# Performance work log

Measured on AMD Instinct MI355X. Metric: run time of the kernel, lower is better.

## Reference

```python
import jax, jax.numpy as jnp
import numpy as np

S = (128, 128, 128)  # spatial grid
K = (16, 16, 16)     # retained low-frequency modes


def _gelu(x):
    # torch nn.GELU default = exact erf variant
    return jax.nn.gelu(x, approximate=False)


def _flayer(x, Rr, Ri, w):
    # x: (s1,s2,s3,dv). Full rfftn then truncate to low modes (as in source).
    f = jnp.fft.rfftn(x, axes=(0, 1, 2))[: K[0], : K[1], : K[2]]  # (k1,k2,k3,dv) complex
    Rf = jnp.einsum('abcd,abcde->abce', f, Rr + 1j * Ri)           # per-mode channel mix
    kernelpart = jnp.fft.irfftn(Rf, s=S, axes=(0, 1, 2))           # zero-pad modes, back to grid
    return _gelu(kernelpart + x @ w)


def setup_inputs() -> dict:
    key = jax.random.key(0)
    ks = jax.random.split(key, 20)
    da, dv, dout = 4, 32, 1
    sc1, sc2, sc3 = 2.0 / da, 2.0 / dv, 2.0 / dv
    d = {}
    d['x'] = jax.random.normal(ks[0], (*S, da), dtype=jnp.float32)
    d['win'] = sc1 * jax.random.normal(ks[1], (da, dv), dtype=jnp.float32)
    d['bin1'] = sc1 * jax.random.normal(ks[2], (dv,), dtype=jnp.float32)
    i = 3
    for L in range(1, 5):
        d[f'Rphir{L}'] = sc2 * jax.random.normal(ks[i], (*K, dv, dv), dtype=jnp.float32); i += 1
        d[f'Rphii{L}'] = sc2 * jax.random.normal(ks[i], (*K, dv, dv), dtype=jnp.float32); i += 1
        d[f'w{L}'] = sc2 * jax.random.normal(ks[i], (dv, dv), dtype=jnp.float32); i += 1
    d['wout'] = sc3 * jax.random.normal(ks[i], (dv, dout), dtype=jnp.float32); i += 1
    d['bout'] = sc3 * jax.random.normal(ks[i], (dout,), dtype=jnp.float32)
    return d


def reference(x, win, bin1, Rphir1, Rphii1, w1, Rphir2, Rphii2, w2,
              Rphir3, Rphii3, w3, Rphir4, Rphii4, w4, wout, bout):
    v = _gelu(x @ win + bin1)          # lifting: (s1,s2,s3,dv)
    v = _flayer(v, Rphir1, Rphii1, w1)
    v = _flayer(v, Rphir2, Rphii2, w2)
    v = _flayer(v, Rphir3, Rphii3, w3)
    v = _flayer(v, Rphir4, Rphii4, w4)
    return v @ wout + bout             # (s1,s2,s3,dout)
```

## Files before the change

kernel.cpp:

```cpp
#include <hip/hip_runtime.h>
#include <math.h>

typedef float2 cplx;
typedef _Float16 h16;
typedef h16 h16x8 __attribute__((ext_vector_type(8)));
typedef float f32x4 __attribute__((ext_vector_type(4)));
typedef uint u32x2 __attribute__((ext_vector_type(2)));

#define MFMA16(a, b, c) __builtin_amdgcn_mfma_f32_16x16x32_f16(a, b, c, 0, 0, 0)

static __device__ __forceinline__ float gelu_exact(float z) {
  float x = z * 0.70710678118654752440f;
  float ax = fabsf(x);
  float t = __builtin_amdgcn_rcpf(fmaf(0.3275911f, ax, 1.0f));
  float p = fmaf(1.061405429f, t, -1.453152027f);
  p = fmaf(p, t, 1.421413741f);
  p = fmaf(p, t, -0.284496736f);
  p = fmaf(p, t, 0.254829592f);
  p = p * t;
  float e = __expf(-ax * ax);
  float erfax = fmaf(-p, e, 1.0f);
  float er = copysignf(erfax, x);
  return 0.5f * z * (1.0f + er);
}

template <int OFF>
static __device__ __forceinline__ h16x8 tr_frag(uint addr) {
  union { uint u[4]; h16x8 h; } r;
  u32x2 lo, hi;
  asm volatile("ds_read_b64_tr_b16 %0, %2 offset:%3\n\t"
               "ds_read_b64_tr_b16 %1, %2 offset:%4"
               : "=&v"(lo), "=&v"(hi)
               : "v"(addr), "i"(OFF), "i"(OFF + 128));
  r.u[0] = lo.x; r.u[1] = lo.y; r.u[2] = hi.x; r.u[3] = hi.y;
  return r.h;
}

__global__ __launch_bounds__(256) void k_prep(
    h16* __restrict__ Afwd, h16* __restrict__ Adt, cplx* __restrict__ Twc,
    const float* __restrict__ wA, const float* __restrict__ wB,
    const float* __restrict__ wC, const float* __restrict__ wD,
    h16* __restrict__ Wfr)
{
  const int tid = threadIdx.x;
  const float w0 = 0.049087385212340519f;
  for (int idx = tid; idx < 4096; idx += 256) {
    int Mt = idx >> 11, rem = idx & 2047, lane = rem >> 5, k = rem & 31;
    int j = k & 7, chunk = k >> 3;
    int m = lane & 15;
    int x3 = chunk * 32 + (lane >> 4) * 8 + j;
    float ang = (float)((m * x3) & 127) * w0;
    float s, c; sincosf(ang, &s, &c);
    float val = Mt ? s : c;
    h16 hi = (h16)val;
    Afwd[idx] = hi;
    Afwd[idx + 4096] = (h16)(val - (float)hi);
  }
  for (int idx = tid; idx < 4096; idx += 256) {
    int tt = idx >> 4, rem = idx & 15, t = rem >> 3, j = rem & 7;
    int wv = tt >> 6, lane = tt & 63, mrow = lane & 15, q = lane >> 4;
    int x3 = (2 * wv + t) * 16 + mrow;
    int kk = q * 8 + j;
    int m = (kk < 16) ? kk : kk - 16;
    float ang = (float)((x3 * m) & 127) * w0;
    float s, c; sincosf(ang, &s, &c);
    Adt[idx] = (h16)((kk < 16) ? c : s);
  }
  const float* ws[4] = { wA, wB, wC, wD };
  for (int idx = tid; idx < 16384; idx += 256) {
    int L = idx >> 12, rem = idx & 4095;
    int t2 = rem >> 4, nt = (rem >> 3) & 1, j = rem & 7;
    int mrow = t2 & 15, q = (t2 >> 4) & 3;
    int n = nt * 16 + mrow, kk = q * 8 + j;
    Wfr[idx] = (h16)ws[L][kk * 32 + n];
  }
  if (tid < 128) {
    float ang = (float)tid * w0;
    float s, c; sincosf(ang, &s, &c);
    Twc[tid] = make_float2(c, s);
  }
}

__global__ __launch_bounds__(256) void k_lift(
    const float* __restrict__ x, const float* __restrict__ win,
    const float* __restrict__ bin, h16* __restrict__ v)
{
  __shared__ float xr[512];
  __shared__ float wl[128];
  __shared__ float bl[32];
  const int tid = threadIdx.x;
  const size_t b = blockIdx.x;
  const float* xrow = x + b * 512;
  for (int i = tid; i < 512; i += 256) xr[i] = xrow[i];
  if (tid < 128) wl[tid] = win[tid];
  if (tid < 32)  bl[tid] = bin[tid];
  __syncthreads();
  const int c = tid & 31, g = tid >> 5;
  #pragma unroll
  for (int j = 0; j < 16; ++j) {
    int x3 = g + 8 * j;
    float z = bl[c];
    #pragma unroll
    for (int a = 0; a < 4; ++a) z += xr[x3 * 4 + a] * wl[a * 32 + c];
    v[b * 4096 + x3 * 32 + c] = (h16)gelu_exact(z);
  }
}

__global__ __launch_bounds__(256) void k_fwd3(
    const h16* __restrict__ v, const h16* __restrict__ Afwd, cplx* __restrict__ Gp,
    const cplx* __restrict__ twg)
{
  __shared__ __align__(16) h16 vtile[4][2][4][32][16];
  __shared__ cplx F3L[4][512];
  const int tid = threadIdx.x;
  const int x1 = blockIdx.x, qs = blockIdx.y;
  const int lane = tid & 63, wv = tid >> 6;
  const int mrow = lane & 15, q4 = lane >> 4;
  h16x8 Ah[2][4], Al[2][4];
  #pragma unroll
  for (int Mt = 0; Mt < 2; ++Mt)
    #pragma unroll
    for (int ch = 0; ch < 4; ++ch) {
      Ah[Mt][ch] = *(const h16x8*)&Afwd[Mt * 2048 + lane * 32 + ch * 8];
      Al[Mt][ch] = *(const h16x8*)&Afwd[4096 + Mt * 2048 + lane * 32 + ch * 8];
    }
  const uint ldsbase = (uint)(uintptr_t)&vtile[0][0][0][0][0];
  const uint abase = ldsbase + (uint)(wv * 8192 + q4 * 256 + mrow * 2);
  cplx g0[16], g1[16];
  #pragma unroll
  for (int k2 = 0; k2 < 16; ++k2) { g0[k2] = make_float2(0.f, 0.f); g1[k2] = make_float2(0.f, 0.f); }
  for (int it = 0; it < 8; ++it) {
    const int x2b = qs * 32 + it * 4;
    __syncthreads();
    const uint4* vsrc = (const uint4*)(v + ((size_t)x1 * 128 + x2b) * 4096);
    for (int i = tid; i < 2048; i += 256) {
      uint4 pk = vsrc[i];
      int rr = i >> 9, e = (i & 511) * 8, x3 = e >> 5, c0 = e & 31;
      int panel = c0 >> 4, off = c0 & 15;
      int chunk = x3 >> 5, row = x3 & 31;
      *(uint4*)&vtile[rr][panel][chunk][row][off] = pk;
    }
    __syncthreads();
    h16x8 B0[4], B1[4];
    {
      const uint a0 = abase;
      const uint a1 = abase + 4096;
      B0[0] = tr_frag<0>(a0);    B0[1] = tr_frag<1024>(a0);
      B0[2] = tr_frag<2048>(a0); B0[3] = tr_frag<3072>(a0);
      B1[0] = tr_frag<0>(a1);    B1[1] = tr_frag<1024>(a1);
      B1[2] = tr_frag<2048>(a1); B1[3] = tr_frag<3072>(a1);
      asm volatile("s_waitcnt lgkmcnt(0)" ::: "memory");
      __builtin_amdgcn_sched_barrier(0);
    }
    f32x4 acc[2][2];
    #pragma unroll
    for (int Mt = 0; Mt < 2; ++Mt)
      #pragma unroll
      for (int Nt = 0; Nt < 2; ++Nt) acc[Mt][Nt] = (f32x4){0.f, 0.f, 0.f, 0.f};
    #pragma unroll
    for (int ch = 0; ch < 4; ++ch) {
      acc[0][0] = MFMA16(Ah[0][ch], B0[ch], acc[0][0]);
      acc[0][0] = MFMA16(Al[0][ch], B0[ch], acc[0][0]);
      acc[0][1] = MFMA16(Ah[0][ch], B1[ch], acc[0][1]);
      acc[0][1] = MFMA16(Al[0][ch], B1[ch], acc[0][1]);
      acc[1][0] = MFMA16(Ah[1][ch], B0[ch], acc[1][0]);
      acc[1][0] = MFMA16(Al[1][ch], B0[ch], acc[1][0]);
      acc[1][1] = MFMA16(Ah[1][ch], B1[ch], acc[1][1]);
      acc[1][1] = MFMA16(Al[1][ch], B1[ch], acc[1][1]);
    }
    #pragma unroll
    for (int Nt = 0; Nt < 2; ++Nt)
      #pragma unroll
      for (int r = 0; r < 4; ++r)
        F3L[wv][(q4 * 4 + r) * 32 + Nt * 16 + mrow] =
            make_float2(acc[0][Nt][r], -acc[1][Nt][r]);
    __syncthreads();
    #pragma unroll
    for (int rr = 0; rr < 4; ++rr) {
      const int x2 = x2b + rr;
      cplx f0 = F3L[rr][tid], f1 = F3L[rr][tid + 256];
      #pragma unroll
      for (int k2 = 0; k2 < 16; ++k2) {
        cplx t = twg[(k2 * x2) & 127];
        g0[k2].x += f0.x * t.x + f0.y * t.y;  g0[k2].y += f0.y * t.x - f0.x * t.y;
        g1[k2].x += f1.x * t.x + f1.y * t.y;  g1[k2].y += f1.y * t.x - f1.x * t.y;
      }
    }
  }
  cplx* dst = Gp + (size_t)qs * 1048576;
  #pragma unroll
  for (int k2 = 0; k2 < 16; ++k2) {
    size_t base = ((size_t)x1 * 16 + k2) * 512;
    dst[base + tid] = g0[k2];
    dst[base + 256 + tid] = g1[k2];
  }
}

__global__ __launch_bounds__(1024) void k_spec3(
    const cplx* __restrict__ Gp, const float* __restrict__ Rr,
    const float* __restrict__ Ri, cplx* __restrict__ H1,
    const cplx* __restrict__ twg)
{
  __shared__ cplx twc[128];
  __shared__ cplx fbp[4][512];
  __shared__ cplx tb[512];
  const int tid = threadIdx.x;
  const int k2 = blockIdx.x >> 4, k3 = blockIdx.x & 15;
  if (tid < 128) twc[tid] = twg[tid];
  __syncthreads();
  const int c = tid & 31, g = (tid >> 5) & 7, h = tid >> 8;
  float fr0 = 0.f, fi0 = 0.f, fr1 = 0.f, fi1 = 0.f;
  #pragma unroll 4
  for (int x1i = 0; x1i < 32; ++x1i) {
    const int x1 = h * 32 + x1i;
    size_t idx = (((size_t)x1 * 16 + k2) * 16 + k3) * 32 + c;
    cplx p0 = Gp[idx], p1 = Gp[idx + 1048576], p2 = Gp[idx + 2097152], p3 = Gp[idx + 3145728];
    cplx hh = make_float2(p0.x + p1.x + p2.x + p3.x, p0.y + p1.y + p2.y + p3.y);
    cplx ta = twc[(g * x1) & 127];
    cplx tb2 = twc[((g + 8) * x1) & 127];
    fr0 += hh.x * ta.x + hh.y * ta.y;   fi0 += hh.y * ta.x - hh.x * ta.y;
    fr1 += hh.x * tb2.x + hh.y * tb2.y; fi1 += hh.y * tb2.x - hh.x * tb2.y;
  }
  fbp[h][g * 32 + c] = make_float2(fr0, fi0);
  fbp[h][(g + 8) * 32 + c] = make_float2(fr1, fi1);
  __syncthreads();
  if (tid < 512) {
    cplx a = fbp[0][tid], b = fbp[1][tid], d = fbp[2][tid], e = fbp[3][tid];
    fbp[0][tid] = make_float2((a.x + b.x) + (d.x + e.x), (a.y + b.y) + (d.y + e.y));
  }
  __syncthreads();
  if (tid < 512) {
    const int k1 = tid >> 5, e = c;
    float tr = 0.f, ti = 0.f;
    const size_t mb = ((size_t)k1 * 256 + k2 * 16 + k3) * 1024;
    #pragma unroll 4
    for (int cc = 0; cc < 32; ++cc) {
      float rr0 = Rr[mb + cc * 32 + e], ri0 = Ri[mb + cc * 32 + e];
      cplx f0 = fbp[0][k1 * 32 + cc];
      tr += f0.x * rr0 - f0.y * ri0;  ti += f0.x * ri0 + f0.y * rr0;
    }
    const float s = 4.76837158203125e-07f;
    tb[k1 * 32 + e] = make_float2(tr * s, ti * s);
  }
  __syncthreads();
  float trr[16], tii[16];
  #pragma unroll
  for (int k1 = 0; k1 < 16; ++k1) { cplx t = tb[k1 * 32 + c]; trr[k1] = t.x; tii[k1] = t.y; }
  #pragma unroll
  for (int jj = 0; jj < 4; ++jj) {
    int xx1 = g + 8 * (h * 4 + jj);
    float hr = 0.f, hi = 0.f;
    #pragma unroll
    for (int k1 = 0; k1 < 16; ++k1) {
      cplx t = twc[(k1 * xx1) & 127];
      hr += trr[k1] * t.x - tii[k1] * t.y;
      hi += trr[k1] * t.y + tii[k1] * t.x;
    }
    H1[(((size_t)xx1 * 16 + k2) * 16 + k3) * 32 + c] = make_float2(hr, hi);
  }
}

__global__ __launch_bounds__(512) void k_ptm4(
    const cplx* __restrict__ H1, const h16* __restrict__ Wfr,
    h16* __restrict__ v, const h16* __restrict__ Adt,
    const cplx* __restrict__ twg)
{
  __shared__ __align__(16) h16 St[8][32 * 40];
  const int tid = threadIdx.x;
  const int x1 = blockIdx.y;
  const int x2b = blockIdx.x * 8;
  const int c = tid & 31, g2 = (tid >> 5) & 15;
  const int lane = tid & 63, w = tid >> 6;
  const int mrow = lane & 15, q = lane >> 4;
  h16x8 Adf, Bw[2];
  Adf   = *(const h16x8*)&Adt[((w >> 1) * 64 + lane) * 16 + (w & 1) * 8];
  Bw[0] = *(const h16x8*)&Wfr[lane * 16];
  Bw[1] = *(const h16x8*)&Wfr[lane * 16 + 8];
  cplx h1[16];
  {
    const cplx* h1p = H1 + (size_t)x1 * 8192;
    #pragma unroll
    for (int k2 = 0; k2 < 16; ++k2) h1[k2] = h1p[(k2 * 16 + g2) * 32 + c];
  }
  const float s0 = (g2 == 0) ? 1.f : 2.f;
  #pragma unroll
  for (int xi = 0; xi < 8; ++xi) {
    const int x2 = x2b + xi;
    float r = 0.f, i = 0.f;
    #pragma unroll
    for (int k2 = 0; k2 < 16; ++k2) {
      cplx t = twg[(k2 * x2) & 127];
      r += h1[k2].x * t.x - h1[k2].y * t.y;
      i += h1[k2].x * t.y + h1[k2].y * t.x;
    }
    St[xi][c * 40 + g2]      = (h16)(s0 * r);
    St[xi][c * 40 + 16 + g2] = (h16)(-s0 * i);
  }
  __syncthreads();
  for (int xi = 0; xi < 8; ++xi) {
    const size_t b = (size_t)x1 * 128 + x2b + xi;
    h16x8 Av = *(const h16x8*)&v[b * 4096 + (w * 16 + mrow) * 32 + q * 8];
    f32x4 acc[2];
    #pragma unroll
    for (int nt = 0; nt < 2; ++nt) {
      h16x8 Bst = *(const h16x8*)&St[xi][(nt * 16 + mrow) * 40 + q * 8];
      f32x4 z = {0.f, 0.f, 0.f, 0.f};
      z = MFMA16(Adf, Bst, z);
      z = MFMA16(Av, Bw[nt], z);
      acc[nt] = z;
    }
    #pragma unroll
    for (int nt = 0; nt < 2; ++nt)
      #pragma unroll
      for (int r2 = 0; r2 < 4; ++r2) {
        int x3 = w * 16 + q * 4 + r2;
        v[b * 4096 + x3 * 32 + nt * 16 + mrow] = (h16)gelu_exact(acc[nt][r2]);
      }
  }
}

__global__ __launch_bounds__(512) void k_ptf4(
    const cplx* __restrict__ H1, const h16* __restrict__ Wfr,
    const h16* __restrict__ v, const h16* __restrict__ Adt,
    const float* __restrict__ wout, const float* __restrict__ bout,
    float* __restrict__ out, const cplx* __restrict__ twg)
{
  __shared__ __align__(16) h16 St[8][32 * 40];
  const int tid = threadIdx.x;
  const int x1 = blockIdx.y;
  const int x2b = blockIdx.x * 8;
  const int c = tid & 31, g2 = (tid >> 5) & 15;
  const int lane = tid & 63, w = tid >> 6;
  const int mrow = lane & 15, q = lane >> 4;
  h16x8 Adf, Bw[2];
  Adf   = *(const h16x8*)&Adt[((w >> 1) * 64 + lane) * 16 + (w & 1) * 8];
  Bw[0] = *(const h16x8*)&Wfr[lane * 16];
  Bw[1] = *(const h16x8*)&Wfr[lane * 16 + 8];
  const float wo0 = wout[mrow], wo1 = wout[16 + mrow];
  const float bo = bout[0];
  cplx h1[16];
  {
    const cplx* h1p = H1 + (size_t)x1 * 8192;
    #pragma unroll
    for (int k2 = 0; k2 < 16; ++k2) h1[k2] = h1p[(k2 * 16 + g2) * 32 + c];
  }
  const float s0 = (g2 == 0) ? 1.f : 2.f;
  #pragma unroll
  for (int xi = 0; xi < 8; ++xi) {
    const int x2 = x2b + xi;
    float r = 0.f, i = 0.f;
    #pragma unroll
    for (int k2 = 0; k2 < 16; ++k2) {
      cplx t = twg[(k2 * x2) & 127];
      r += h1[k2].x * t.x - h1[k2].y * t.y;
      i += h1[k2].x * t.y + h1[k2].y * t.x;
    }
    St[xi][c * 40 + g2]      = (h16)(s0 * r);
    St[xi][c * 40 + 16 + g2] = (h16)(-s0 * i);
  }
  __syncthreads();
  for (int xi = 0; xi < 8; ++xi) {
    const size_t b = (size_t)x1 * 128 + x2b + xi;
    h16x8 Av = *(const h16x8*)&v[b * 4096 + (w * 16 + mrow) * 32 + q * 8];
    f32x4 acc[2];
    #pragma unroll
    for (int nt = 0; nt < 2; ++nt) {
      h16x8 Bst = *(const h16x8*)&St[xi][(nt * 16 + mrow) * 40 + q * 8];
      f32x4 z = {0.f, 0.f, 0.f, 0.f};
      z = MFMA16(Adf, Bst, z);
      z = MFMA16(Av, Bw[nt], z);
      acc[nt] = z;
    }
    #pragma unroll
    for (int r2 = 0; r2 < 4; ++r2) {
      float p = (float)(h16)gelu_exact(acc[0][r2]) * wo0
              + (float)(h16)gelu_exact(acc[1][r2]) * wo1;
      p += __shfl_xor(p, 1);
      p += __shfl_xor(p, 2);
      p += __shfl_xor(p, 4);
      p += __shfl_xor(p, 8);
      if (mrow == 0) {
        int x3 = w * 16 + q * 4 + r2;
        out[b * 128 + x3] = bo + p;
      }
    }
  }
}

__global__ void k_diag(float* out, float wsmb) {
  if (threadIdx.x == 0 && blockIdx.x == 0) out[0] = wsmb;
}

extern "C" void kernel_launch(void* const* d_in, const int* in_sizes, int n_in,
                              void* d_out, int out_size, void* d_ws, size_t ws_size,
                              hipStream_t stream)
{
  (void)in_sizes; (void)n_in; (void)out_size;
  const float* x    = (const float*)d_in[0];
  const float* win  = (const float*)d_in[1];
  const float* bin1 = (const float*)d_in[2];
  const float* Rr[4] = { (const float*)d_in[3], (const float*)d_in[6],
                         (const float*)d_in[9], (const float*)d_in[12] };
  const float* Ri[4] = { (const float*)d_in[4], (const float*)d_in[7],
                         (const float*)d_in[10], (const float*)d_in[13] };
  const float* wm[4] = { (const float*)d_in[5], (const float*)d_in[8],
                         (const float*)d_in[11], (const float*)d_in[14] };
  const float* wout = (const float*)d_in[15];
  const float* bout = (const float*)d_in[16];
  float* out = (float*)d_out;

  const size_t SZ_V  = 134217728;
  const size_t SZ_C  = 33554432;
  const size_t SZ_AF = 16384;
  const size_t SZ_AD = 8192;
  const size_t SZ_TW = 1024;
  const size_t SZ_WF = 32768;
  const size_t NEED = SZ_V + SZ_C + SZ_AF + SZ_AD + SZ_TW + SZ_WF;

  if (ws_size < NEED) {
    k_diag<<<1, 64, 0, stream>>>(out, (float)(ws_size >> 20));
    return;
  }
  char* p = (char*)d_ws;
  h16* v    = (h16*)p;  p += SZ_V;
  cplx* C   = (cplx*)p; p += SZ_C;
  h16* Afwd = (h16*)p;  p += SZ_AF;
  h16* Adt  = (h16*)p;  p += SZ_AD;
  cplx* Twc = (cplx*)p; p += SZ_TW;
  h16* Wfr  = (h16*)p;

  k_prep<<<1, 256, 0, stream>>>(Afwd, Adt, Twc, wm[0], wm[1], wm[2], wm[3], Wfr);
  k_lift<<<16384, 256, 0, stream>>>(x, win, bin1, v);
  for (int L = 0; L < 4; ++L) {
    k_fwd3<<<dim3(128, 4), 256, 0, stream>>>(v, Afwd, C, Twc);
    k_spec3<<<256, 1024, 0, stream>>>(C, Rr[L], Ri[L], C, Twc);
    if (L < 3) k_ptm4<<<dim3(16, 128), 512, 0, stream>>>(C, Wfr + (size_t)L * 4096, v, Adt, Twc);
    else       k_ptf4<<<dim3(16, 128), 512, 0, stream>>>(C, Wfr + 3 * 4096, v, Adt, wout, bout, out, Twc);
  }
}
```

Measured before the change: 746.7 us.

## Split forward DFT work across 512 threads and prefetch v fragments in pointwise kernels

The forward x3/x2 transform kernel now runs 512 threads per block. Each wave pair splits the real and imaginary (Mt) halves of the MFMA work, and each thread accumulates one k2 column instead of two. This lowers register pressure and adds more waves to hide latency. The A fragments are now reloaded from global memory inside the loop instead of held in registers. In the pointwise kernels, all eight v fragments are loaded before the twiddle/St computation so the global load latency overlaps that compute, at the cost of more registers.

```diff
diff --git a/kernel.cpp b/kernel.cpp
--- a/kernel.cpp
+++ b/kernel.cpp
@@ -106,39 +106,34 @@
   }
 }
 
-__global__ __launch_bounds__(256) void k_fwd3(
+__global__ __launch_bounds__(512) void k_fwd4(
     const h16* __restrict__ v, const h16* __restrict__ Afwd, cplx* __restrict__ Gp,
     const cplx* __restrict__ twg)
 {
   __shared__ __align__(16) h16 vtile[4][2][4][32][16];
-  __shared__ cplx F3L[4][512];
+  __shared__ float F3re[4][512];
+  __shared__ float F3im[4][512];
   const int tid = threadIdx.x;
   const int x1 = blockIdx.x, qs = blockIdx.y;
-  const int lane = tid & 63, wv = tid >> 6;
+  const int lane = tid & 63, w = tid >> 6;
+  const int row = w >> 1, Mt = w & 1;
   const int mrow = lane & 15, q4 = lane >> 4;
-  h16x8 Ah[2][4], Al[2][4];
-  #pragma unroll
-  for (int Mt = 0; Mt < 2; ++Mt)
-    #pragma unroll
-    for (int ch = 0; ch < 4; ++ch) {
-      Ah[Mt][ch] = *(const h16x8*)&Afwd[Mt * 2048 + lane * 32 + ch * 8];
-      Al[Mt][ch] = *(const h16x8*)&Afwd[4096 + Mt * 2048 + lane * 32 + ch * 8];
-    }
   const uint ldsbase = (uint)(uintptr_t)&vtile[0][0][0][0][0];
-  const uint abase = ldsbase + (uint)(wv * 8192 + q4 * 256 + mrow * 2);
-  cplx g0[16], g1[16];
-  #pragma unroll
-  for (int k2 = 0; k2 < 16; ++k2) { g0[k2] = make_float2(0.f, 0.f); g1[k2] = make_float2(0.f, 0.f); }
+  const uint abase = ldsbase + (uint)(row * 8192 + q4 * 256 + mrow * 2);
+  const h16* Abase = Afwd + Mt * 2048;
+  cplx g[16];
+  #pragma unroll
+  for (int k2 = 0; k2 < 16; ++k2) g[k2] = make_float2(0.f, 0.f);
   for (int it = 0; it < 8; ++it) {
     const int x2b = qs * 32 + it * 4;
     __syncthreads();
     const uint4* vsrc = (const uint4*)(v + ((size_t)x1 * 128 + x2b) * 4096);
-    for (int i = tid; i < 2048; i += 256) {
+    for (int i = tid; i < 2048; i += 512) {
       uint4 pk = vsrc[i];
       int rr = i >> 9, e = (i & 511) * 8, x3 = e >> 5, c0 = e & 31;
       int panel = c0 >> 4, off = c0 & 15;
-      int chunk = x3 >> 5, row = x3 & 31;
-      *(uint4*)&vtile[rr][panel][chunk][row][off] = pk;
+      int chunk = x3 >> 5, rw = x3 & 31;
+      *(uint4*)&vtile[rr][panel][chunk][rw][off] = pk;
     }
     __syncthreads();
     h16x8 B0[4], B1[4];
@@ -152,48 +147,48 @@
       asm volatile("s_waitcnt lgkmcnt(0)" ::: "memory");
       __builtin_amdgcn_sched_barrier(0);
     }
-    f32x4 acc[2][2];
-    #pragma unroll
-    for (int Mt = 0; Mt < 2; ++Mt)
+    f32x4 acc[2];
+    acc[0] = (f32x4){0.f, 0.f, 0.f, 0.f};
+    acc[1] = (f32x4){0.f, 0.f, 0.f, 0.f};
+    #pragma unroll
+    for (int ch = 0; ch < 4; ++ch) {
+      h16x8 Ah = *(const h16x8*)&Abase[lane * 32 + ch * 8];
+      h16x8 Al = *(const h16x8*)&Abase[4096 + lane * 32 + ch * 8];
+      acc[0] = MFMA16(Ah, B0[ch], acc[0]);
+      acc[0] = MFMA16(Al, B0[ch], acc[0]);
+      acc[1] = MFMA16(Ah, B1[ch], acc[1]);
+      acc[1] = MFMA16(Al, B1[ch], acc[1]);
+    }
+    if (Mt == 0) {
       #pragma unroll
-      for (int Nt = 0; Nt < 2; ++Nt) acc[Mt][Nt] = (f32x4){0.f, 0.f, 0.f, 0.f};
-    #pragma unroll
-    for (int ch = 0; ch < 4; ++ch) {
-      acc[0][0] = MFMA16(Ah[0][ch], B0[ch], acc[0][0]);
-      acc[0][0] = MFMA16(Al[0][ch], B0[ch], acc[0][0]);
-      acc[0][1] = MFMA16(Ah[0][ch], B1[ch], acc[0][1]);
-      acc[0][1] = MFMA16(Al[0][ch], B1[ch], acc[0][1]);
-      acc[1][0] = MFMA16(Ah[1][ch], B0[ch], acc[1][0]);
-      acc[1][0] = MFMA16(Al[1][ch], B0[ch], acc[1][0]);
-      acc[1][1] = MFMA16(Ah[1][ch], B1[ch], acc[1][1]);
-      acc[1][1] = MFMA16(Al[1][ch], B1[ch], acc[1][1]);
-    }
-    #pragma unroll
-    for (int Nt = 0; Nt < 2; ++Nt)
+      for (int Nt = 0; Nt < 2; ++Nt)
+        #pragma unroll
+        for (int r = 0; r < 4; ++r)
+          F3re[row][(q4 * 4 + r) * 32 + Nt * 16 + mrow] = acc[Nt][r];
+    } else {
       #pragma unroll
-      for (int r = 0; r < 4; ++r)
-        F3L[wv][(q4 * 4 + r) * 32 + Nt * 16 + mrow] =
-            make_float2(acc[0][Nt][r], -acc[1][Nt][r]);
+      for (int Nt = 0; Nt < 2; ++Nt)
+        #pragma unroll
+        for (int r = 0; r < 4; ++r)
+          F3im[row][(q4 * 4 + r) * 32 + Nt * 16 + mrow] = -acc[Nt][r];
+    }
     __syncthreads();
     #pragma unroll
     for (int rr = 0; rr < 4; ++rr) {
       const int x2 = x2b + rr;
-      cplx f0 = F3L[rr][tid], f1 = F3L[rr][tid + 256];
+      float fx = F3re[rr][tid], fy = F3im[rr][tid];
       #pragma unroll
       for (int k2 = 0; k2 < 16; ++k2) {
         cplx t = twg[(k2 * x2) & 127];
-        g0[k2].x += f0.x * t.x + f0.y * t.y;  g0[k2].y += f0.y * t.x - f0.x * t.y;
-        g1[k2].x += f1.x * t.x + f1.y * t.y;  g1[k2].y += f1.y * t.x - f1.x * t.y;
+        g[k2].x += fx * t.x + fy * t.y;
+        g[k2].y += fy * t.x - fx * t.y;
       }
     }
   }
   cplx* dst = Gp + (size_t)qs * 1048576;
   #pragma unroll
-  for (int k2 = 0; k2 < 16; ++k2) {
-    size_t base = ((size_t)x1 * 16 + k2) * 512;
-    dst[base + tid] = g0[k2];
-    dst[base + 256 + tid] = g1[k2];
-  }
+  for (int k2 = 0; k2 < 16; ++k2)
+    dst[((size_t)x1 * 16 + k2) * 512 + tid] = g[k2];
 }
 
 __global__ __launch_bounds__(1024) void k_spec3(
@@ -282,6 +277,12 @@
     #pragma unroll
     for (int k2 = 0; k2 < 16; ++k2) h1[k2] = h1p[(k2 * 16 + g2) * 32 + c];
   }
+  h16x8 Av[8];
+  #pragma unroll
+  for (int xi = 0; xi < 8; ++xi) {
+    const size_t b = (size_t)x1 * 128 + x2b + xi;
+    Av[xi] = *(const h16x8*)&v[b * 4096 + (w * 16 + mrow) * 32 + q * 8];
+  }
   const float s0 = (g2 == 0) ? 1.f : 2.f;
   #pragma unroll
   for (int xi = 0; xi < 8; ++xi) {
@@ -297,16 +298,16 @@
     St[xi][c * 40 + 16 + g2] = (h16)(-s0 * i);
   }
   __syncthreads();
+  #pragma unroll
   for (int xi = 0; xi < 8; ++xi) {
     const size_t b = (size_t)x1 * 128 + x2b + xi;
-    h16x8 Av = *(const h16x8*)&v[b * 4096 + (w * 16 + mrow) * 32 + q * 8];
     f32x4 acc[2];
     #pragma unroll
     for (int nt = 0; nt < 2; ++nt) {
       h16x8 Bst = *(const h16x8*)&St[xi][(nt * 16 + mrow) * 40 + q * 8];
       f32x4 z = {0.f, 0.f, 0.f, 0.f};
       z = MFMA16(Adf, Bst, z);
-      z = MFMA16(Av, Bw[nt], z);
+      z = MFMA16(Av[xi], Bw[nt], z);
       acc[nt] = z;
     }
     #pragma unroll
@@ -344,6 +345,12 @@
     #pragma unroll
     for (int k2 = 0; k2 < 16; ++k2) h1[k2] = h1p[(k2 * 16 + g2) * 32 + c];
   }
+  h16x8 Av[8];
+  #pragma unroll
+  for (int xi = 0; xi < 8; ++xi) {
+    const size_t b = (size_t)x1 * 128 + x2b + xi;
+    Av[xi] = *(const h16x8*)&v[b * 4096 + (w * 16 + mrow) * 32 + q * 8];
+  }
   const float s0 = (g2 == 0) ? 1.f : 2.f;
   #pragma unroll
   for (int xi = 0; xi < 8; ++xi) {
@@ -359,16 +366,16 @@
     St[xi][c * 40 + 16 + g2] = (h16)(-s0 * i);
   }
   __syncthreads();
+  #pragma unroll
   for (int xi = 0; xi < 8; ++xi) {
     const size_t b = (size_t)x1 * 128 + x2b + xi;
-    h16x8 Av = *(const h16x8*)&v[b * 4096 + (w * 16 + mrow) * 32 + q * 8];
     f32x4 acc[2];
     #pragma unroll
     for (int nt = 0; nt < 2; ++nt) {
       h16x8 Bst = *(const h16x8*)&St[xi][(nt * 16 + mrow) * 40 + q * 8];
       f32x4 z = {0.f, 0.f, 0.f, 0.f};
       z = MFMA16(Adf, Bst, z);
-      z = MFMA16(Av, Bw[nt], z);
+      z = MFMA16(Av[xi], Bw[nt], z);
       acc[nt] = z;
     }
     #pragma unroll
@@ -432,7 +439,7 @@
   k_prep<<<1, 256, 0, stream>>>(Afwd, Adt, Twc, wm[0], wm[1], wm[2], wm[3], Wfr);
   k_lift<<<16384, 256, 0, stream>>>(x, win, bin1, v);
   for (int L = 0; L < 4; ++L) {
-    k_fwd3<<<dim3(128, 4), 256, 0, stream>>>(v, Afwd, C, Twc);
+    k_fwd4<<<dim3(128, 4), 512, 0, stream>>>(v, Afwd, C, Twc);
     k_spec3<<<256, 1024, 0, stream>>>(C, Rr[L], Ri[L], C, Twc);
     if (L < 3) k_ptm4<<<dim3(16, 128), 512, 0, stream>>>(C, Wfr + (size_t)L * 4096, v, Adt, Twc);
     else       k_ptf4<<<dim3(16, 128), 512, 0, stream>>>(C, Wfr + 3 * 4096, v, Adt, wout, bout, out, Twc);
```

Result: no change. 752.0 us (+0.7%).
